# Optimization experiments

Measured on AMD Instinct MI355X. Metric: run time of the kernel, lower is better.

Reference implementation:

```python
import jax, jax.numpy as jnp
import numpy as np
import math

BLOCK_SIZE = 64
GATE_HIDDEN = 128


def _rmsnorm(x, w, eps=1e-6):
    v = jnp.mean(jnp.square(x), axis=-1, keepdims=True)
    return x * jax.lax.rsqrt(v + eps) * w


def _rotate_half(x):
    x1, x2 = jnp.split(x, 2, axis=-1)
    return jnp.concatenate([-x2, x1], axis=-1)


def _rope(x, cos, sin):
    # x: [B, S, H, D]; cos/sin: [B, S, D] -> unsqueeze head dim (unsqueeze_dim=2)
    c = cos[:, :, None, :]
    s = sin[:, :, None, :]
    return x * c + _rotate_half(x) * s


def setup_inputs() -> dict:
    key = jax.random.key(0)
    ks = jax.random.split(key, 10)
    B, S, Hk, D = 4, 65536, 8, 128
    Hq, g, Dg = 32, 4, GATE_HIDDEN
    nb = S // BLOCK_SIZE
    xav_q = math.sqrt(6.0 / (D + Dg))
    xav_k = math.sqrt(6.0 / (2 * D + Dg))
    return {
        "k": jax.random.normal(ks[0], (B, S, Hk, D), jnp.float32),
        "q": jax.random.normal(ks[1], (B, 1, Hq, D), jnp.float32),
        "Wq": jax.random.uniform(ks[2], (Hk, g, D, Dg), jnp.float32, -xav_q, xav_q),
        "Wk": jax.random.uniform(ks[3], (Hk, 2 * D, Dg), jnp.float32, -xav_k, xav_k),
        "qnorm_w": jnp.ones((Dg,), jnp.float32),
        "knorm_w": jnp.ones((Dg,), jnp.float32),
        "cos_q": jax.random.uniform(ks[4], (B, 1, Dg), jnp.float32, -1.0, 1.0),
        "sin_q": jax.random.uniform(ks[5], (B, 1, Dg), jnp.float32, -1.0, 1.0),
        "cos_k": jax.random.uniform(ks[6], (B, nb, Dg), jnp.float32, -1.0, 1.0),
        "sin_k": jax.random.uniform(ks[7], (B, nb, Dg), jnp.float32, -1.0, 1.0),
        "attention_mask": jnp.ones((B, Hk, nb), jnp.bool_),
        "block_budget": 128,
    }


def reference(k, q, Wq, Wk, qnorm_w, knorm_w, cos_q, sin_q, cos_k, sin_k,
              attention_mask, block_budget):
    B, S, Hk, D = k.shape
    nb = S // BLOCK_SIZE
    g = q.shape[2] // Hk
    Dg = Wk.shape[-1]
    scale = 1.0 / math.sqrt(Dg)

    # --- K path: block pooling (avg + max) -> per-head linear -> RMSNorm -> RoPE
    kb = k.reshape(B, nb, BLOCK_SIZE, Hk, D)
    k_pooled = jnp.concatenate([kb.mean(axis=2), kb.max(axis=2)], axis=-1)  # [B,nb,Hk,2D]
    k_c = jnp.einsum('bshi,hio->bsho', k_pooled, Wk)                         # [B,nb,Hk,Dg]
    k_c = _rmsnorm(k_c, knorm_w)
    k_c = _rope(k_c, cos_k, sin_k)

    # --- Q path (Qproj): grouped per-k-head projection -> RMSNorm -> RoPE
    qg = q.reshape(B, 1, Hk, g, D)
    qp = jnp.einsum('bskgi,kgio->bsko', qg, Wq)                              # [B,1,Hk,Dg]
    qp = _rmsnorm(qp, qnorm_w)
    qp = _rope(qp, cos_q, sin_q)
    qv = qp[:, 0]                                                            # [B,Hk,Dg]

    # --- gate scores + softmax
    attn = jnp.einsum('bhd,bshd->bhs', qv, k_c) * scale                      # [B,Hk,nb]
    attn = jnp.where(attention_mask, attn, jnp.float32(-1e20))
    attn = jax.nn.softmax(attn, axis=-1)

    # --- token_budget sparse block mask: topk + scatter
    _, topk_idx = jax.lax.top_k(attn, block_budget)                          # [B,Hk,k]
    blk = jnp.arange(nb)
    mask = jnp.any(topk_idx[..., :, None] == blk[None, None, None, :], axis=-2)
    mask = mask & attention_mask
    mask = mask.at[:, :, -1].set(True)
    return mask
```

## Files before the change

### kernel.cpp

```cpp
#include <hip/hip_runtime.h>
#include <hip/hip_bf16.h>
#include <math.h>

#define NB   1024
#define HKH  8

typedef float f4 __attribute__((ext_vector_type(4)));

__global__ __launch_bounds__(512) void qproj_kernel(const float* __restrict__ q,
                                                    const float* __restrict__ Wq,
                                                    const float* __restrict__ qnw,
                                                    const float* __restrict__ cq,
                                                    const float* __restrict__ sq,
                                                    float* __restrict__ qv) {
    int b = blockIdx.x >> 3, h = blockIdx.x & 7;
    int t = threadIdx.x;
    int o = t & 127, seg = t >> 7;
    __shared__ float qs[512];
    __shared__ float part[4][128];
    __shared__ float red[2];
    __shared__ float ybuf[128];
    qs[t] = q[(size_t)b * 4096 + (size_t)h * 512 + t];
    __syncthreads();
    const float* wqp = Wq + (size_t)h * 512 * 128 + o;
    float acc = 0.0f;
    int g0 = seg * 128;
#pragma unroll 4
    for (int gi = g0; gi < g0 + 128; ++gi)
        acc = fmaf(qs[gi], wqp[(size_t)gi * 128], acc);
    part[seg][o] = acc;
    __syncthreads();
    if (t < 128) {
        float a = part[0][o] + part[1][o] + part[2][o] + part[3][o];
        ybuf[o] = a;
        float ss = a * a;
        for (int off = 32; off > 0; off >>= 1) ss += __shfl_xor(ss, off);
        if ((o & 63) == 0) red[o >> 6] = ss;
    }
    __syncthreads();
    if (t < 128) {
        float scale = rsqrtf((red[0] + red[1]) * (1.0f / 128.0f) + 1e-6f);
        float y  = ybuf[o] * scale * qnw[o];
        int op   = (o < 64) ? o + 64 : o - 64;
        float yp = ybuf[op] * scale * qnw[op];
        float rot = (o < 64) ? -yp : yp;
        qv[((size_t)b * HKH + h) * 128 + o] =
            fmaf(y, cq[b * 128 + o], rot * sq[b * 128 + o]);
    }
}

__global__ __launch_bounds__(256) void fused_kernel(const float* __restrict__ kin,
                                                    const float* __restrict__ Wk,
                                                    const float* __restrict__ knw,
                                                    const float* __restrict__ cosk,
                                                    const float* __restrict__ sink,
                                                    const float* __restrict__ qv,
                                                    float* __restrict__ scores) {
    __shared__ float At[256][17];
    __shared__ float Ws[64][128];
    int wg   = blockIdx.x;
    int tile = wg & 63;
    int h    = (wg >> 6) & 7;
    int b    = wg >> 9;
    int t    = threadIdx.x;

    {
        int f4lane = t & 31;
        int halfw  = t >> 5;
        const float inv = 1.0f / 64.0f;
#pragma unroll
        for (int bi = 0; bi < 2; ++bi) {
            int blk = halfw * 2 + bi;
            size_t s0 = (size_t)b * 65536 + ((size_t)tile * 16 + blk) * 64;
            const f4* src = (const f4*)(kin + s0 * 1024 + (size_t)h * 128) + f4lane;
            f4 v = __builtin_nontemporal_load(src);
            f4 s = v, m = v;
#pragma unroll 8
            for (int r = 1; r < 64; ++r) {
                f4 u = __builtin_nontemporal_load(src + (size_t)r * 256);
                s += u;
                m.x = fmaxf(m.x, u.x); m.y = fmaxf(m.y, u.y);
                m.z = fmaxf(m.z, u.z); m.w = fmaxf(m.w, u.w);
            }
            int k0 = f4lane * 4;
            At[k0 + 0][blk] = s.x * inv; At[k0 + 1][blk] = s.y * inv;
            At[k0 + 2][blk] = s.z * inv; At[k0 + 3][blk] = s.w * inv;
            At[128 + k0 + 0][blk] = m.x; At[128 + k0 + 1][blk] = m.y;
            At[128 + k0 + 2][blk] = m.z; At[128 + k0 + 3][blk] = m.w;
        }
    }

    int tc = t & 15, tr = t >> 4;
    float acc[8];
#pragma unroll
    for (int j = 0; j < 8; ++j) acc[j] = 0.0f;

    for (int kk = 0; kk < 256; kk += 64) {
        __syncthreads();
#pragma unroll
        for (int ii = 0; ii < 8; ++ii) {
            int idx = t + ii * 256;
            int kw = idx >> 5, c4 = idx & 31;
            *(f4*)&Ws[kw][c4 * 4] =
                *(const f4*)(Wk + ((size_t)h * 256 + kk + kw) * 128 + c4 * 4);
        }
        __syncthreads();
#pragma unroll
        for (int k = 0; k < 64; ++k) {
            float a = At[kk + k][tr];
            f4 wlo = *(const f4*)&Ws[k][tc * 4];
            f4 whi = *(const f4*)&Ws[k][64 + tc * 4];
            acc[0] = fmaf(a, wlo.x, acc[0]);
            acc[1] = fmaf(a, wlo.y, acc[1]);
            acc[2] = fmaf(a, wlo.z, acc[2]);
            acc[3] = fmaf(a, wlo.w, acc[3]);
            acc[4] = fmaf(a, whi.x, acc[4]);
            acc[5] = fmaf(a, whi.y, acc[5]);
            acc[6] = fmaf(a, whi.z, acc[6]);
            acc[7] = fmaf(a, whi.w, acc[7]);
        }
    }

    int blkg = tile * 16 + tr;
    float ss = 0.0f;
#pragma unroll
    for (int j = 0; j < 8; ++j) ss = fmaf(acc[j], acc[j], ss);
#pragma unroll
    for (int off = 1; off < 16; off <<= 1) ss += __shfl_xor(ss, off);
    float scale = rsqrtf(ss * (1.0f / 128.0f) + 1e-6f);
    const float* cb  = cosk + ((size_t)b * NB + blkg) * 128;
    const float* sb  = sink + ((size_t)b * NB + blkg) * 128;
    const float* qvp = qv + ((size_t)b * HKH + h) * 128;
    float part = 0.0f;
#pragma unroll
    for (int j = 0; j < 4; ++j) {
        int olo = tc * 4 + j, ohi = 64 + olo;
        float ylo = acc[j]     * scale * knw[olo];
        float yhi = acc[4 + j] * scale * knw[ohi];
        float zlo = fmaf(ylo, cb[olo], -(yhi * sb[olo]));
        float zhi = fmaf(yhi, cb[ohi],  ylo * sb[ohi]);
        part = fmaf(zlo, qvp[olo], part);
        part = fmaf(zhi, qvp[ohi], part);
    }
#pragma unroll
    for (int off = 1; off < 16; off <<= 1) part += __shfl_xor(part, off);
    if (tc == 0)
        scores[((size_t)b * HKH + h) * NB + blkg] = part * 0.08838834764831845f;
}

__device__ inline bool read_mask(const void* amp, int mode, size_t idx) {
    if (mode == 1) return ((const int*)amp)[idx] != 0;
    if (mode == 2) return ((const unsigned int*)amp)[idx] != 0u;
    return ((const unsigned char*)amp)[idx] != 0;
}

__global__ __launch_bounds__(512) void topk_kernel(const float* __restrict__ scores,
                                                   const void* __restrict__ amraw,
                                                   const int* __restrict__ bbp,
                                                   int* __restrict__ out) {
    int b = blockIdx.x >> 3, h = blockIdx.x & 7;
    int t = threadIdx.x;
    __shared__ float sv[NB];
    __shared__ int mode_sh;

    if (t == 0) {
        const unsigned int* w = (const unsigned int*)amraw;
        bool allint = true, allflt = true;
        for (int i = 0; i < 64; ++i) {
            unsigned int x = w[i];
            if (x != 0u && x != 1u) allint = false;
            if (x != 0u && x != 0x3f800000u) allflt = false;
        }
        mode_sh = allint ? 1 : (allflt ? 2 : 0);
    }
    __syncthreads();
    int mode = mode_sh;
    size_t rowoff = ((size_t)b * HKH + h) * NB;
    const float* src = scores + rowoff;
    for (int s = t; s < NB; s += 512)
        sv[s] = read_mask(amraw, mode, rowoff + s) ? src[s] : -1e20f;
    __syncthreads();

    int bb = bbp[0];
    if (bb > NB) bb = NB;
    if (bb < 1)  bb = 1;

    int e0 = t, e1 = t + 512;
    float v0 = sv[e0], v1 = sv[e1];
    int r0 = 0, r1 = 0;
#pragma unroll 4
    for (int j4 = 0; j4 < 256; ++j4) {
        f4 w = *(const f4*)&sv[j4 * 4];
        int jb = j4 * 4;
        r0 += (w.x > v0) + (w.y > v0) + (w.z > v0) + (w.w > v0);
        r1 += (w.x > v1) + (w.y > v1) + (w.z > v1) + (w.w > v1);
        r0 += (w.x == v0 && jb + 0 < e0) + (w.y == v0 && jb + 1 < e0)
            + (w.z == v0 && jb + 2 < e0) + (w.w == v0 && jb + 3 < e0);
        r1 += (w.x == v1 && jb + 0 < e1) + (w.y == v1 && jb + 1 < e1)
            + (w.z == v1 && jb + 2 < e1) + (w.w == v1 && jb + 3 < e1);
    }
    int* dst = out + rowoff;
    bool am0 = read_mask(amraw, mode, rowoff + e0);
    bool am1 = read_mask(amraw, mode, rowoff + e1);
    dst[e0] = ((r0 < bb && am0)) ? 1 : 0;
    dst[e1] = ((r1 < bb && am1) || (e1 == NB - 1)) ? 1 : 0;
}

extern "C" void kernel_launch(void* const* d_in, const int* in_sizes, int n_in,
                              void* d_out, int out_size, void* d_ws, size_t ws_size,
                              hipStream_t stream) {
    (void)in_sizes; (void)n_in; (void)out_size; (void)ws_size;
    const float* k   = (const float*)d_in[0];
    const float* q   = (const float*)d_in[1];
    const float* Wq  = (const float*)d_in[2];
    const float* Wk  = (const float*)d_in[3];
    const float* qnw = (const float*)d_in[4];
    const float* knw = (const float*)d_in[5];
    const float* cq  = (const float*)d_in[6];
    const float* sq  = (const float*)d_in[7];
    const float* ck  = (const float*)d_in[8];
    const float* sk  = (const float*)d_in[9];
    const void*  am  = d_in[10];
    const int*   bb  = (const int*)d_in[11];
    int* out = (int*)d_out;

    float* qv     = (float*)d_ws;
    float* scores = qv + 4 * HKH * 128;

    qproj_kernel<<<32, 512, 0, stream>>>(q, Wq, qnw, cq, sq, qv);
    fused_kernel<<<2048, 256, 0, stream>>>(k, Wk, knw, ck, sk, qv, scores);
    topk_kernel<<<32, 512, 0, stream>>>(scores, am, bb, out);
}
```

Before: 264.2 us.

## Fuse Q projection into pooling kernel and retile Wk GEMM to 32 blocks

Result: slower. 311.6 us (+18.0%).

```diff
diff --git a/kernel.cpp b/kernel.cpp
--- a/kernel.cpp
+++ b/kernel.cpp
@@ -7,72 +7,63 @@
 
 typedef float f4 __attribute__((ext_vector_type(4)));
 
-__global__ __launch_bounds__(512) void qproj_kernel(const float* __restrict__ q,
+__global__ __launch_bounds__(256) void fused_kernel(const float* __restrict__ kin,
+                                                    const float* __restrict__ qrow,
                                                     const float* __restrict__ Wq,
+                                                    const float* __restrict__ Wk,
                                                     const float* __restrict__ qnw,
+                                                    const float* __restrict__ knw,
                                                     const float* __restrict__ cq,
                                                     const float* __restrict__ sq,
-                                                    float* __restrict__ qv) {
-    int b = blockIdx.x >> 3, h = blockIdx.x & 7;
-    int t = threadIdx.x;
-    int o = t & 127, seg = t >> 7;
-    __shared__ float qs[512];
-    __shared__ float part[4][128];
-    __shared__ float red[2];
-    __shared__ float ybuf[128];
-    qs[t] = q[(size_t)b * 4096 + (size_t)h * 512 + t];
-    __syncthreads();
-    const float* wqp = Wq + (size_t)h * 512 * 128 + o;
-    float acc = 0.0f;
-    int g0 = seg * 128;
-#pragma unroll 4
-    for (int gi = g0; gi < g0 + 128; ++gi)
-        acc = fmaf(qs[gi], wqp[(size_t)gi * 128], acc);
-    part[seg][o] = acc;
-    __syncthreads();
-    if (t < 128) {
-        float a = part[0][o] + part[1][o] + part[2][o] + part[3][o];
-        ybuf[o] = a;
-        float ss = a * a;
-        for (int off = 32; off > 0; off >>= 1) ss += __shfl_xor(ss, off);
-        if ((o & 63) == 0) red[o >> 6] = ss;
-    }
-    __syncthreads();
-    if (t < 128) {
-        float scale = rsqrtf((red[0] + red[1]) * (1.0f / 128.0f) + 1e-6f);
-        float y  = ybuf[o] * scale * qnw[o];
-        int op   = (o < 64) ? o + 64 : o - 64;
-        float yp = ybuf[op] * scale * qnw[op];
-        float rot = (o < 64) ? -yp : yp;
-        qv[((size_t)b * HKH + h) * 128 + o] =
-            fmaf(y, cq[b * 128 + o], rot * sq[b * 128 + o]);
-    }
-}
-
-__global__ __launch_bounds__(256) void fused_kernel(const float* __restrict__ kin,
-                                                    const float* __restrict__ Wk,
-                                                    const float* __restrict__ knw,
                                                     const float* __restrict__ cosk,
                                                     const float* __restrict__ sink,
-                                                    const float* __restrict__ qv,
                                                     float* __restrict__ scores) {
-    __shared__ float At[256][17];
-    __shared__ float Ws[64][128];
+    __shared__ float At[256][36];
+    __shared__ float qs[512];
     int wg   = blockIdx.x;
-    int tile = wg & 63;
-    int h    = (wg >> 6) & 7;
-    int b    = wg >> 9;
+    int tile = wg & 31;
+    int h    = (wg >> 5) & 7;
+    int b    = wg >> 8;
     int t    = threadIdx.x;
-
+    int tc   = t & 31;
+    int tr   = t >> 5;
+
+    qs[t]       = qrow[(size_t)b * 4096 + (size_t)h * 512 + t];
+    qs[t + 256] = qrow[(size_t)b * 4096 + (size_t)h * 512 + t + 256];
+    __syncthreads();
+    float qv[4];
     {
-        int f4lane = t & 31;
-        int halfw  = t >> 5;
+        const float* wq = Wq + (size_t)h * 512 * 128 + tc * 4;
+        float aq[4] = {0.f, 0.f, 0.f, 0.f};
+#pragma unroll 4
+        for (int gi = 0; gi < 512; ++gi) {
+            f4 w = *(const f4*)(wq + (size_t)gi * 128);
+            float qg = qs[gi];
+            aq[0] = fmaf(qg, w.x, aq[0]); aq[1] = fmaf(qg, w.y, aq[1]);
+            aq[2] = fmaf(qg, w.z, aq[2]); aq[3] = fmaf(qg, w.w, aq[3]);
+        }
+        float ss = aq[0]*aq[0] + aq[1]*aq[1] + aq[2]*aq[2] + aq[3]*aq[3];
+#pragma unroll
+        for (int off = 1; off < 32; off <<= 1) ss += __shfl_xor(ss, off);
+        float scale = rsqrtf(ss * (1.0f / 128.0f) + 1e-6f);
+#pragma unroll
+        for (int j = 0; j < 4; ++j) {
+            int o = tc * 4 + j;
+            float y  = aq[j] * scale * qnw[o];
+            float yp = __shfl_xor(y, 16);
+            float rot = (tc < 16) ? -yp : yp;
+            qv[j] = fmaf(y, cq[b * 128 + o], rot * sq[b * 128 + o]);
+        }
+    }
+    __syncthreads();
+
+    {
         const float inv = 1.0f / 64.0f;
 #pragma unroll
-        for (int bi = 0; bi < 2; ++bi) {
-            int blk = halfw * 2 + bi;
-            size_t s0 = (size_t)b * 65536 + ((size_t)tile * 16 + blk) * 64;
-            const f4* src = (const f4*)(kin + s0 * 1024 + (size_t)h * 128) + f4lane;
+        for (int bi = 0; bi < 4; ++bi) {
+            int blk = tr * 4 + bi;
+            size_t row0 = (size_t)b * 65536 + ((size_t)tile * 32 + blk) * 64;
+            const f4* src = (const f4*)(kin + row0 * 1024 + (size_t)h * 128) + tc;
             f4 v = __builtin_nontemporal_load(src);
             f4 s = v, m = v;
 #pragma unroll 8
@@ -82,70 +73,64 @@
                 m.x = fmaxf(m.x, u.x); m.y = fmaxf(m.y, u.y);
                 m.z = fmaxf(m.z, u.z); m.w = fmaxf(m.w, u.w);
             }
-            int k0 = f4lane * 4;
+            int k0 = tc * 4;
             At[k0 + 0][blk] = s.x * inv; At[k0 + 1][blk] = s.y * inv;
             At[k0 + 2][blk] = s.z * inv; At[k0 + 3][blk] = s.w * inv;
             At[128 + k0 + 0][blk] = m.x; At[128 + k0 + 1][blk] = m.y;
             At[128 + k0 + 2][blk] = m.z; At[128 + k0 + 3][blk] = m.w;
         }
     }
-
-    int tc = t & 15, tr = t >> 4;
-    float acc[8];
-#pragma unroll
-    for (int j = 0; j < 8; ++j) acc[j] = 0.0f;
-
-    for (int kk = 0; kk < 256; kk += 64) {
-        __syncthreads();
-#pragma unroll
-        for (int ii = 0; ii < 8; ++ii) {
-            int idx = t + ii * 256;
-            int kw = idx >> 5, c4 = idx & 31;
-            *(f4*)&Ws[kw][c4 * 4] =
-                *(const f4*)(Wk + ((size_t)h * 256 + kk + kw) * 128 + c4 * 4);
-        }
-        __syncthreads();
-#pragma unroll
-        for (int k = 0; k < 64; ++k) {
-            float a = At[kk + k][tr];
-            f4 wlo = *(const f4*)&Ws[k][tc * 4];
-            f4 whi = *(const f4*)&Ws[k][64 + tc * 4];
-            acc[0] = fmaf(a, wlo.x, acc[0]);
-            acc[1] = fmaf(a, wlo.y, acc[1]);
-            acc[2] = fmaf(a, wlo.z, acc[2]);
-            acc[3] = fmaf(a, wlo.w, acc[3]);
-            acc[4] = fmaf(a, whi.x, acc[4]);
-            acc[5] = fmaf(a, whi.y, acc[5]);
-            acc[6] = fmaf(a, whi.z, acc[6]);
-            acc[7] = fmaf(a, whi.w, acc[7]);
-        }
-    }
-
-    int blkg = tile * 16 + tr;
-    float ss = 0.0f;
-#pragma unroll
-    for (int j = 0; j < 8; ++j) ss = fmaf(acc[j], acc[j], ss);
-#pragma unroll
-    for (int off = 1; off < 16; off <<= 1) ss += __shfl_xor(ss, off);
-    float scale = rsqrtf(ss * (1.0f / 128.0f) + 1e-6f);
-    const float* cb  = cosk + ((size_t)b * NB + blkg) * 128;
-    const float* sb  = sink + ((size_t)b * NB + blkg) * 128;
-    const float* qvp = qv + ((size_t)b * HKH + h) * 128;
-    float part = 0.0f;
-#pragma unroll
-    for (int j = 0; j < 4; ++j) {
-        int olo = tc * 4 + j, ohi = 64 + olo;
-        float ylo = acc[j]     * scale * knw[olo];
-        float yhi = acc[4 + j] * scale * knw[ohi];
-        float zlo = fmaf(ylo, cb[olo], -(yhi * sb[olo]));
-        float zhi = fmaf(yhi, cb[ohi],  ylo * sb[ohi]);
-        part = fmaf(zlo, qvp[olo], part);
-        part = fmaf(zhi, qvp[ohi], part);
-    }
-#pragma unroll
-    for (int off = 1; off < 16; off <<= 1) part += __shfl_xor(part, off);
-    if (tc == 0)
-        scores[((size_t)b * HKH + h) * NB + blkg] = part * 0.08838834764831845f;
+    __syncthreads();
+
+    float acc[4][4];
+#pragma unroll
+    for (int i = 0; i < 4; ++i)
+#pragma unroll
+        for (int j = 0; j < 4; ++j) acc[i][j] = 0.0f;
+    const float* Wb = Wk + (size_t)h * 256 * 128 + tc * 4;
+#pragma unroll 8
+    for (int k = 0; k < 256; ++k) {
+        f4 a = *(const f4*)&At[k][tr * 4];
+        f4 w = *(const f4*)(Wb + (size_t)k * 128);
+        acc[0][0] = fmaf(a.x, w.x, acc[0][0]); acc[0][1] = fmaf(a.x, w.y, acc[0][1]);
+        acc[0][2] = fmaf(a.x, w.z, acc[0][2]); acc[0][3] = fmaf(a.x, w.w, acc[0][3]);
+        acc[1][0] = fmaf(a.y, w.x, acc[1][0]); acc[1][1] = fmaf(a.y, w.y, acc[1][1]);
+        acc[1][2] = fmaf(a.y, w.z, acc[1][2]); acc[1][3] = fmaf(a.y, w.w, acc[1][3]);
+        acc[2][0] = fmaf(a.z, w.x, acc[2][0]); acc[2][1] = fmaf(a.z, w.y, acc[2][1]);
+        acc[2][2] = fmaf(a.z, w.z, acc[2][2]); acc[2][3] = fmaf(a.z, w.w, acc[2][3]);
+        acc[3][0] = fmaf(a.w, w.x, acc[3][0]); acc[3][1] = fmaf(a.w, w.y, acc[3][1]);
+        acc[3][2] = fmaf(a.w, w.z, acc[3][2]); acc[3][3] = fmaf(a.w, w.w, acc[3][3]);
+    }
+
+    float kn[4];
+#pragma unroll
+    for (int j = 0; j < 4; ++j) kn[j] = knw[tc * 4 + j];
+#pragma unroll
+    for (int i = 0; i < 4; ++i) {
+        int blkg = tile * 32 + tr * 4 + i;
+        float ss = 0.0f;
+#pragma unroll
+        for (int j = 0; j < 4; ++j) ss = fmaf(acc[i][j], acc[i][j], ss);
+#pragma unroll
+        for (int off = 1; off < 32; off <<= 1) ss += __shfl_xor(ss, off);
+        float scale = rsqrtf(ss * (1.0f / 128.0f) + 1e-6f);
+        const float* cb = cosk + ((size_t)b * NB + blkg) * 128;
+        const float* sb = sink + ((size_t)b * NB + blkg) * 128;
+        float part = 0.0f;
+#pragma unroll
+        for (int j = 0; j < 4; ++j) {
+            int o = tc * 4 + j;
+            float y  = acc[i][j] * scale * kn[j];
+            float yp = __shfl_xor(y, 16);
+            float rot = (tc < 16) ? -yp : yp;
+            float z = fmaf(y, cb[o], rot * sb[o]);
+            part = fmaf(z, qv[j], part);
+        }
+#pragma unroll
+        for (int off = 1; off < 32; off <<= 1) part += __shfl_xor(part, off);
+        if (tc == 0)
+            scores[((size_t)b * HKH + h) * NB + blkg] = part * 0.08838834764831845f;
+    }
 }
 
 __device__ inline bool read_mask(const void* amp, int mode, size_t idx) {
@@ -224,10 +209,9 @@
     const int*   bb  = (const int*)d_in[11];
     int* out = (int*)d_out;
 
-    float* qv     = (float*)d_ws;
-    float* scores = qv + 4 * HKH * 128;
-
-    qproj_kernel<<<32, 512, 0, stream>>>(q, Wq, qnw, cq, sq, qv);
-    fused_kernel<<<2048, 256, 0, stream>>>(k, Wk, knw, ck, sk, qv, scores);
+    float* scores = (float*)d_ws;
+
+    fused_kernel<<<1024, 256, 0, stream>>>(k, q, Wq, Wk, qnw, knw,
+                                           cq, sq, ck, sk, scores);
     topk_kernel<<<32, 512, 0, stream>>>(scores, am, bb, out);
 }
```

## Restructure fused pooling+GEMM: 32 blocks per workgroup, Wk from global, swizzled LDS

Applied to the files above, without the earlier changes.

Measured after the change: 285.7 us. 1.08x slower.

```diff
diff --git a/kernel.cpp b/kernel.cpp
--- a/kernel.cpp
+++ b/kernel.cpp
@@ -56,23 +56,22 @@
                                                     const float* __restrict__ sink,
                                                     const float* __restrict__ qv,
                                                     float* __restrict__ scores) {
-    __shared__ float At[256][17];
-    __shared__ float Ws[64][128];
+    __shared__ float At[32][256];
     int wg   = blockIdx.x;
-    int tile = wg & 63;
-    int h    = (wg >> 6) & 7;
-    int b    = wg >> 9;
+    int h    = wg & 7;
+    int tile = (wg >> 3) & 31;
+    int b    = wg >> 8;
     int t    = threadIdx.x;
 
     {
-        int f4lane = t & 31;
-        int halfw  = t >> 5;
+        int tc = t & 31;
+        int tr = t >> 5;
         const float inv = 1.0f / 64.0f;
 #pragma unroll
-        for (int bi = 0; bi < 2; ++bi) {
-            int blk = halfw * 2 + bi;
-            size_t s0 = (size_t)b * 65536 + ((size_t)tile * 16 + blk) * 64;
-            const f4* src = (const f4*)(kin + s0 * 1024 + (size_t)h * 128) + f4lane;
+        for (int bi = 0; bi < 4; ++bi) {
+            int blk = tr * 4 + bi;
+            size_t row0 = (size_t)b * 65536 + ((size_t)tile * 32 + blk) * 64;
+            const f4* src = (const f4*)(kin + row0 * 1024 + (size_t)h * 128) + tc;
             f4 v = __builtin_nontemporal_load(src);
             f4 s = v, m = v;
 #pragma unroll 8
@@ -82,70 +81,73 @@
                 m.x = fmaxf(m.x, u.x); m.y = fmaxf(m.y, u.y);
                 m.z = fmaxf(m.z, u.z); m.w = fmaxf(m.w, u.w);
             }
-            int k0 = f4lane * 4;
-            At[k0 + 0][blk] = s.x * inv; At[k0 + 1][blk] = s.y * inv;
-            At[k0 + 2][blk] = s.z * inv; At[k0 + 3][blk] = s.w * inv;
-            At[128 + k0 + 0][blk] = m.x; At[128 + k0 + 1][blk] = m.y;
-            At[128 + k0 + 2][blk] = m.z; At[128 + k0 + 3][blk] = m.w;
-        }
-    }
-
-    int tc = t & 15, tr = t >> 4;
-    float acc[8];
-#pragma unroll
-    for (int j = 0; j < 8; ++j) acc[j] = 0.0f;
-
-    for (int kk = 0; kk < 256; kk += 64) {
-        __syncthreads();
-#pragma unroll
-        for (int ii = 0; ii < 8; ++ii) {
-            int idx = t + ii * 256;
-            int kw = idx >> 5, c4 = idx & 31;
-            *(f4*)&Ws[kw][c4 * 4] =
-                *(const f4*)(Wk + ((size_t)h * 256 + kk + kw) * 128 + c4 * 4);
-        }
-        __syncthreads();
-#pragma unroll
-        for (int k = 0; k < 64; ++k) {
-            float a = At[kk + k][tr];
-            f4 wlo = *(const f4*)&Ws[k][tc * 4];
-            f4 whi = *(const f4*)&Ws[k][64 + tc * 4];
-            acc[0] = fmaf(a, wlo.x, acc[0]);
-            acc[1] = fmaf(a, wlo.y, acc[1]);
-            acc[2] = fmaf(a, wlo.z, acc[2]);
-            acc[3] = fmaf(a, wlo.w, acc[3]);
-            acc[4] = fmaf(a, whi.x, acc[4]);
-            acc[5] = fmaf(a, whi.y, acc[5]);
-            acc[6] = fmaf(a, whi.z, acc[6]);
-            acc[7] = fmaf(a, whi.w, acc[7]);
-        }
-    }
-
-    int blkg = tile * 16 + tr;
-    float ss = 0.0f;
-#pragma unroll
-    for (int j = 0; j < 8; ++j) ss = fmaf(acc[j], acc[j], ss);
-#pragma unroll
-    for (int off = 1; off < 16; off <<= 1) ss += __shfl_xor(ss, off);
-    float scale = rsqrtf(ss * (1.0f / 128.0f) + 1e-6f);
-    const float* cb  = cosk + ((size_t)b * NB + blkg) * 128;
-    const float* sb  = sink + ((size_t)b * NB + blkg) * 128;
-    const float* qvp = qv + ((size_t)b * HKH + h) * 128;
-    float part = 0.0f;
-#pragma unroll
-    for (int j = 0; j < 4; ++j) {
-        int olo = tc * 4 + j, ohi = 64 + olo;
-        float ylo = acc[j]     * scale * knw[olo];
-        float yhi = acc[4 + j] * scale * knw[ohi];
-        float zlo = fmaf(ylo, cb[olo], -(yhi * sb[olo]));
-        float zhi = fmaf(yhi, cb[ohi],  ylo * sb[ohi]);
-        part = fmaf(zlo, qvp[olo], part);
-        part = fmaf(zhi, qvp[ohi], part);
-    }
-#pragma unroll
-    for (int off = 1; off < 16; off <<= 1) part += __shfl_xor(part, off);
-    if (tc == 0)
-        scores[((size_t)b * HKH + h) * NB + blkg] = part * 0.08838834764831845f;
+            int sw = blk & 7;
+            f4 mean = { s.x * inv, s.y * inv, s.z * inv, s.w * inv };
+            *(f4*)&At[blk][(tc ^ sw) << 2]        = mean;
+            *(f4*)&At[blk][((tc + 32) ^ sw) << 2] = m;
+        }
+    }
+    __syncthreads();
+
+    int cg = t & 15;
+    int rg = t >> 4;
+    int r0 = rg * 2, r1 = r0 + 1;
+    int s0 = r0 & 7, s1 = r1 & 7;
+    float acc0[8], acc1[8];
+#pragma unroll
+    for (int j = 0; j < 8; ++j) { acc0[j] = 0.0f; acc1[j] = 0.0f; }
+    const float* Wb = Wk + (size_t)h * 256 * 128 + cg * 8;
+#pragma unroll 2
+    for (int kq = 0; kq < 64; ++kq) {
+        f4 a0 = *(const f4*)&At[r0][(kq ^ s0) << 2];
+        f4 a1 = *(const f4*)&At[r1][(kq ^ s1) << 2];
+        const float* wrow = Wb + (size_t)kq * 512;
+#pragma unroll
+        for (int dk = 0; dk < 4; ++dk) {
+            f4 w0 = *(const f4*)(wrow + dk * 128);
+            f4 w1 = *(const f4*)(wrow + dk * 128 + 4);
+            float av0 = a0[dk], av1 = a1[dk];
+            acc0[0] = fmaf(av0, w0.x, acc0[0]); acc0[1] = fmaf(av0, w0.y, acc0[1]);
+            acc0[2] = fmaf(av0, w0.z, acc0[2]); acc0[3] = fmaf(av0, w0.w, acc0[3]);
+            acc0[4] = fmaf(av0, w1.x, acc0[4]); acc0[5] = fmaf(av0, w1.y, acc0[5]);
+            acc0[6] = fmaf(av0, w1.z, acc0[6]); acc0[7] = fmaf(av0, w1.w, acc0[7]);
+            acc1[0] = fmaf(av1, w0.x, acc1[0]); acc1[1] = fmaf(av1, w0.y, acc1[1]);
+            acc1[2] = fmaf(av1, w0.z, acc1[2]); acc1[3] = fmaf(av1, w0.w, acc1[3]);
+            acc1[4] = fmaf(av1, w1.x, acc1[4]); acc1[5] = fmaf(av1, w1.y, acc1[5]);
+            acc1[6] = fmaf(av1, w1.z, acc1[6]); acc1[7] = fmaf(av1, w1.w, acc1[7]);
+        }
+    }
+
+    float kn[8], qvr[8];
+    const float* qvp = qv + ((size_t)b * HKH + h) * 128 + cg * 8;
+#pragma unroll
+    for (int j = 0; j < 8; ++j) { kn[j] = knw[cg * 8 + j]; qvr[j] = qvp[j]; }
+#pragma unroll
+    for (int i = 0; i < 2; ++i) {
+        float* acc = i ? acc1 : acc0;
+        int blkg = tile * 32 + r0 + i;
+        float ss = 0.0f;
+#pragma unroll
+        for (int j = 0; j < 8; ++j) ss = fmaf(acc[j], acc[j], ss);
+#pragma unroll
+        for (int off = 1; off < 16; off <<= 1) ss += __shfl_xor(ss, off);
+        float scale = rsqrtf(ss * (1.0f / 128.0f) + 1e-6f);
+        const float* cb = cosk + ((size_t)b * NB + blkg) * 128 + cg * 8;
+        const float* sb = sink + ((size_t)b * NB + blkg) * 128 + cg * 8;
+        float part = 0.0f;
+#pragma unroll
+        for (int j = 0; j < 8; ++j) {
+            float y  = acc[j] * scale * kn[j];
+            float yp = __shfl_xor(y, 8);
+            float rot = (cg < 8) ? -yp : yp;
+            float z = fmaf(y, cb[j], rot * sb[j]);
+            part = fmaf(z, qvr[j], part);
+        }
+#pragma unroll
+        for (int off = 1; off < 16; off <<= 1) part += __shfl_xor(part, off);
+        if (cg == 0)
+            scores[((size_t)b * HKH + h) * NB + blkg] = part * 0.08838834764831845f;
+    }
 }
 
 __device__ inline bool read_mask(const void* amp, int mode, size_t idx) {
@@ -228,6 +230,6 @@
     float* scores = qv + 4 * HKH * 128;
 
     qproj_kernel<<<32, 512, 0, stream>>>(q, Wq, qnw, cq, sq, qv);
-    fused_kernel<<<2048, 256, 0, stream>>>(k, Wk, knw, ck, sk, qv, scores);
+    fused_kernel<<<1024, 256, 0, stream>>>(k, Wk, knw, ck, sk, qv, scores);
     topk_kernel<<<32, 512, 0, stream>>>(scores, am, bb, out);
 }
```
